# Optimization experiments

Measured on AMD Instinct MI355X. Metric: run time of the kernel, lower is better.

## Reference

```python
import jax, jax.numpy as jnp
import numpy as np

N, E, D, H, L, FF = 50000, 500000, 128, 8, 2, 512
HD = D // H  # head dim = 16


def setup_inputs() -> dict:
    key = jax.random.key(0)
    ks = jax.random.split(key, 16)
    inp = {
        "x": jax.random.normal(ks[0], (N, D), jnp.float32),
        "edge_index": jax.random.randint(ks[1], (2, E), 0, N, jnp.int32),
    }
    def w(k, shape, fan_in):
        return jax.random.normal(k, shape, jnp.float32) / np.float32(np.sqrt(fan_in))
    inp["Wq"] = w(ks[2], (L, D, D), D)
    inp["Wk"] = w(ks[3], (L, D, D), D)
    inp["Wv"] = w(ks[4], (L, D, D), D)
    inp["Wo"] = w(ks[5], (L, D, D), D)
    inp["Wpos"] = w(ks[6], (L, D, D), D)
    inp["Wdeg"] = w(ks[7], (L, 1, D), 1)
    inp["W1"] = w(ks[8], (L, D, FF), D)
    inp["W2"] = w(ks[9], (L, FF, D), FF)
    for name, shape in [("bq", (L, D)), ("bk", (L, D)), ("bv", (L, D)),
                        ("bo", (L, D)), ("bpos", (L, D)), ("bdeg", (L, D)),
                        ("ln1_b", (L, D)), ("ln2_b", (L, D)),
                        ("b1", (L, FF)), ("b2", (L, D))]:
        inp[name] = jnp.zeros(shape, jnp.float32)
    inp["ln1_g"] = jnp.ones((L, D), jnp.float32)
    inp["ln2_g"] = jnp.ones((L, D), jnp.float32)
    return inp


def _layernorm(x, g, b):
    mu = jnp.mean(x, axis=-1, keepdims=True)
    var = jnp.mean(jnp.square(x - mu), axis=-1, keepdims=True)
    return (x - mu) * jax.lax.rsqrt(var + 1e-5) * g + b


def _forward(edge_index, x, Wq, bq, Wk, bk, Wv, bv, Wo, bo, Wpos, bpos,
             Wdeg, bdeg, ln1_g, ln1_b, ln2_g, ln2_b, W1, b1, W2, b2):
    n = x.shape[0]
    loops = jnp.arange(n, dtype=edge_index.dtype)
    src = jnp.concatenate([edge_index[0], loops])  # [E+N]
    dst = jnp.concatenate([edge_index[1], loops])  # [E+N]
    scale = np.float32(np.sqrt(HD))
    for l in range(L):
        # pre-attention LayerNorm
        xn = _layernorm(x, ln1_g[l], ln1_b[l])
        # positional encoding: x + proj(x) + deg_proj(standardized degree)
        deg = jax.ops.segment_sum(jnp.ones_like(src, dtype=x.dtype), src, num_segments=n)
        deg = (deg - deg.mean()) / (jnp.std(deg, ddof=1) + 1e-6)
        pos = xn @ Wpos[l] + bpos[l] + deg[:, None] * Wdeg[l][0] + bdeg[l]
        xp = xn + pos
        # per-node QKV projections (linear => identical to per-edge projection)
        q = (xp @ Wq[l] + bq[l]).reshape(n, H, HD)
        k = (xp @ Wk[l] + bk[l]).reshape(n, H, HD)
        v = (xp @ Wv[l] + bv[l]).reshape(n, H, HD)
        # per-edge attention logits  [E+N, H]
        att = jnp.einsum('ehd,ehd->eh', q[dst], k[src]) / scale
        att = jnp.nan_to_num(jnp.clip(att, -50.0, 50.0), nan=0.0, posinf=50.0, neginf=-50.0)
        # segment softmax over destination nodes (every node has a self loop)
        m = jax.ops.segment_max(att, dst, num_segments=n)        # [N, H]
        ex = jnp.exp(att - m[dst])
        s = jax.ops.segment_sum(ex, dst, num_segments=n)
        alpha = ex / (s[dst] + 1e-16)                             # [E+N, H]
        # weighted aggregation + output projection
        msg = (v[src] * alpha[:, :, None]).reshape(-1, D)         # [E+N, D]
        aggr = jax.ops.segment_sum(msg, dst, num_segments=n)      # [N, D]
        x = x + (aggr @ Wo[l] + bo[l])
        # FFN sublayer
        h = jax.nn.gelu(_layernorm(x, ln2_g[l], ln2_b[l]) @ W1[l] + b1[l], approximate=False)
        x = x + (h @ W2[l] + b2[l])
    return x


def reference(x, edge_index, Wq, bq, Wk, bk, Wv, bv, Wo, bo, Wpos, bpos,
              Wdeg, bdeg, ln1_g, ln1_b, ln2_g, ln2_b, W1, b1, W2, b2):
    return _forward(edge_index, x, Wq, bq, Wk, bk, Wv, bv, Wo, bo, Wpos, bpos,
                    Wdeg, bdeg, ln1_g, ln1_b, ln2_g, ln2_b, W1, b1, W2, b2)
```

## Files before the change

### kernel.cpp

```cpp
#include <hip/hip_runtime.h>
#include <hip/hip_bf16.h>
#include <hip/hip_fp16.h>
#include <math.h>

#define DMODEL 128
#define NHEAD 8
#define HEADD 16
#define NLAYER 2
#define FFDIM 512
#define MPAD 50048
#define QKVW 384
#define CSTRIDE 128
#define LSTR 134

using short8 = __attribute__((ext_vector_type(8))) short;
using half8  = __attribute__((ext_vector_type(8))) _Float16;
using f32x4  = __attribute__((ext_vector_type(4))) float;

static __device__ __forceinline__ unsigned short f2h(float f) {
    __half h = __float2half(f);
    unsigned short u; __builtin_memcpy(&u, &h, 2); return u;
}
static __device__ __forceinline__ float h2f(unsigned short u) {
    __half h; __builtin_memcpy(&h, &u, 2); return __half2float(h);
}
static __device__ __forceinline__ half8 s2h8(short8 s) {
    half8 h; __builtin_memcpy(&h, &s, 16); return h;
}
static __device__ __forceinline__ f32x4 MFMAH(short8 a, short8 b, f32x4 c) {
    return __builtin_amdgcn_mfma_f32_16x16x32_f16(s2h8(a), s2h8(b), c, 0, 0, 0);
}
static __device__ __forceinline__ float gelu_fast(float v) {
    float u = v * (0.7978845608f + 0.0356774081f * v * v);
    float t = 1.0f - 2.0f / (1.0f + __expf(2.0f * u));
    return 0.5f * v * (1.0f + t);
}

__global__ __launch_bounds__(256)
void mega_setup(const int* __restrict__ ei, float* __restrict__ deg,
                int* __restrict__ cnt, int* __restrict__ csr2, int e, int n, int nbT,
                const float* __restrict__ Wq, const float* __restrict__ Wk,
                const float* __restrict__ Wv, const float* __restrict__ Wo,
                const float* __restrict__ Wpos, const float* __restrict__ W1,
                const float* __restrict__ W2,
                unsigned short* __restrict__ wqkvt, unsigned short* __restrict__ wot,
                unsigned short* __restrict__ wpt, unsigned short* __restrict__ w1t,
                unsigned short* __restrict__ w2t, int nbW,
                const float* __restrict__ x_in, const float* __restrict__ g1,
                const float* __restrict__ b1, unsigned short* __restrict__ xnb)
{
    const int bid = blockIdx.x;
    if (bid < nbT) {
        int i = bid * 256 + threadIdx.x;
        if (i < e) {
            int s = ei[i], d = ei[e + i];
            atomicAdd(&deg[s], 1.0f);
            int pos = atomicAdd(&cnt[d], 1);
            if (pos < CSTRIDE) csr2[(size_t)d * CSTRIDE + pos] = s;
        } else if (i < e + n) {
            int d = i - e;
            int pos = atomicAdd(&cnt[d], 1);
            if (pos < CSTRIDE) csr2[(size_t)d * CSTRIDE + pos] = d;
        }
    } else if (bid < nbT + nbW) {
        const int DD = NLAYER * DMODEL * DMODEL;
        const int DF = NLAYER * DMODEL * FFDIM;
        int i = (bid - nbT) * 256 + threadIdx.x;
        if (i < 3 * DD) {
            int w = i / DD, r = i - w * DD;
            const float* src = (w == 0) ? Wq : (w == 1 ? Wk : Wv);
            int l = r >> 14, rr = r & 16383;
            int k = rr >> 7, nn = rr & 127;
            wqkvt[(size_t)l * QKVW * DMODEL + (size_t)(w * 128 + nn) * DMODEL + k] = f2h(src[r]);
        } else if (i < 5 * DD) {
            int w = (i - 3 * DD) / DD, r = (i - 3 * DD) - w * DD;
            const float* src = (w == 0) ? Wo : Wpos;
            unsigned short* dst = (w == 0) ? wot : wpt;
            int l = r >> 14, rr = r & 16383;
            int k = rr >> 7, nn = rr & 127;
            dst[(size_t)l * DMODEL * DMODEL + (size_t)nn * DMODEL + k] = f2h(src[r]);
        } else if (i < 5 * DD + DF) {
            int r = i - 5 * DD;
            int l = r >> 16, rr = r & 65535;
            int k = rr >> 9, nn = rr & 511;
            w1t[(size_t)l * FFDIM * DMODEL + (size_t)nn * DMODEL + k] = f2h(W1[r]);
        } else if (i < 5 * DD + 2 * DF) {
            int r = i - 5 * DD - DF;
            int l = r >> 16, rr = r & 65535;
            int k = rr >> 7, nn = rr & 127;
            w2t[(size_t)l * DMODEL * FFDIM + (size_t)nn * FFDIM + k] = f2h(W2[r]);
        }
    } else {
        int wave = threadIdx.x >> 6;
        int lane = threadIdx.x & 63;
        int row  = (bid - nbT - nbW) * 4 + wave;
        if (row >= n) return;
        float2 xv = *(const float2*)(x_in + (size_t)row * DMODEL + lane * 2);
        float s  = xv.x + xv.y;
        float ss = xv.x * xv.x + xv.y * xv.y;
        #pragma unroll
        for (int d = 1; d < 64; d <<= 1) {
            s  += __shfl_xor(s, d);
            ss += __shfl_xor(ss, d);
        }
        float mu   = s * (1.0f / 128.0f);
        float var  = ss * (1.0f / 128.0f) - mu * mu;
        float rstd = rsqrtf(var + 1e-5f);
        float2 gv = *(const float2*)(g1 + lane * 2);
        float2 bv = *(const float2*)(b1 + lane * 2);
        ushort2 o;
        o.x = f2h((xv.x - mu) * rstd * gv.x + bv.x);
        o.y = f2h((xv.y - mu) * rstd * gv.y + bv.y);
        *(ushort2*)(xnb + (size_t)row * DMODEL + lane * 2) = o;
    }
}

__global__ __launch_bounds__(256)
void deg_var(const float* __restrict__ deg, float* __restrict__ stats, float mean, int n)
{
    float acc = 0.f;
    for (int i = blockIdx.x * blockDim.x + threadIdx.x; i < n; i += gridDim.x * blockDim.x) {
        float d = (deg[i] + 1.0f) - mean;
        acc += d * d;
    }
    #pragma unroll
    for (int d = 1; d < 64; d <<= 1) acc += __shfl_xor(acc, d);
    __shared__ float wsum[4];
    int lane = threadIdx.x & 63, wv = threadIdx.x >> 6;
    if (lane == 0) wsum[wv] = acc;
    __syncthreads();
    if (threadIdx.x == 0) atomicAdd(stats, wsum[0] + wsum[1] + wsum[2] + wsum[3]);
}

static __device__ __forceinline__ void ep_resln(
    f32x4 (&acc)[2][4], float* sm, int row0,
    int wr, int wc, int quad, int l15,
    const float* __restrict__ bias, const float* __restrict__ g,
    const float* __restrict__ bb,
    float* __restrict__ x, unsigned short* __restrict__ lnout, int n)
{
    #pragma unroll
    for (int i = 0; i < 2; ++i) {
        #pragma unroll
        for (int rr = 0; rr < 4; ++rr) {
            int rl = wr * 32 + i * 16 + quad * 4 + rr;
            size_t gr = (size_t)row0 + rl;
            float ps = 0.f, pq = 0.f;
            #pragma unroll
            for (int j = 0; j < 4; ++j) {
                int gc = wc * 64 + j * 16 + l15;
                float xv = (gr < (size_t)n) ? x[gr * DMODEL + gc] : 0.f;
                float v = acc[i][j][rr] + bias[gc] + xv;
                acc[i][j][rr] = v;
                ps += v; pq += v * v;
            }
            ps += __shfl_xor(ps, 1); pq += __shfl_xor(pq, 1);
            ps += __shfl_xor(ps, 2); pq += __shfl_xor(pq, 2);
            ps += __shfl_xor(ps, 4); pq += __shfl_xor(pq, 4);
            ps += __shfl_xor(ps, 8); pq += __shfl_xor(pq, 8);
            if (l15 == 0) { sm[(rl * 2 + wc) * 2 + 0] = ps; sm[(rl * 2 + wc) * 2 + 1] = pq; }
        }
    }
    __syncthreads();
    #pragma unroll
    for (int i = 0; i < 2; ++i) {
        #pragma unroll
        for (int rr = 0; rr < 4; ++rr) {
            int rl = wr * 32 + i * 16 + quad * 4 + rr;
            size_t gr = (size_t)row0 + rl;
            if (gr >= (size_t)n) continue;
            float su = sm[(rl * 2 + 0) * 2 + 0] + sm[(rl * 2 + 1) * 2 + 0];
            float sq = sm[(rl * 2 + 0) * 2 + 1] + sm[(rl * 2 + 1) * 2 + 1];
            float mu   = su * (1.f / 128.f);
            float var  = sq * (1.f / 128.f) - mu * mu;
            float rstd = rsqrtf(var + 1e-5f);
            #pragma unroll
            for (int j = 0; j < 4; ++j) {
                int gc = wc * 64 + j * 16 + l15;
                float v = acc[i][j][rr];
                x[gr * DMODEL + gc] = v;
                lnout[gr * DMODEL + gc] = f2h((v - mu) * rstd * g[gc] + bb[gc]);
            }
        }
    }
}

static __device__ __forceinline__ void ep_resln_lds(
    f32x4 (&acc)[2][4], float* sm, int row0,
    int wr, int wc, int quad, int l15,
    const float* __restrict__ bias, const float* __restrict__ g,
    const float* __restrict__ bb,
    float* __restrict__ x, unsigned short* AsLds, int n)
{
    #pragma unroll
    for (int i = 0; i < 2; ++i) {
        #pragma unroll
        for (int rr = 0; rr < 4; ++rr) {
            int rl = wr * 32 + i * 16 + quad * 4 + rr;
            size_t gr = (size_t)row0 + rl;
            float ps = 0.f, pq = 0.f;
            #pragma unroll
            for (int j = 0; j < 4; ++j) {
                int gc = wc * 64 + j * 16 + l15;
                float xv = (gr < (size_t)n) ? x[gr * DMODEL + gc] : 0.f;
                float v = acc[i][j][rr] + bias[gc] + xv;
                acc[i][j][rr] = v;
                ps += v; pq += v * v;
            }
            ps += __shfl_xor(ps, 1); pq += __shfl_xor(pq, 1);
            ps += __shfl_xor(ps, 2); pq += __shfl_xor(pq, 2);
            ps += __shfl_xor(ps, 4); pq += __shfl_xor(pq, 4);
            ps += __shfl_xor(ps, 8); pq += __shfl_xor(pq, 8);
            if (l15 == 0) { sm[(rl * 2 + wc) * 2 + 0] = ps; sm[(rl * 2 + wc) * 2 + 1] = pq; }
        }
    }
    __syncthreads();
    #pragma unroll
    for (int i = 0; i < 2; ++i) {
        #pragma unroll
        for (int rr = 0; rr < 4; ++rr) {
            int rl = wr * 32 + i * 16 + quad * 4 + rr;
            size_t gr = (size_t)row0 + rl;
            if (gr >= (size_t)n) continue;
            float su = sm[(rl * 2 + 0) * 2 + 0] + sm[(rl * 2 + 1) * 2 + 0];
            float sq = sm[(rl * 2 + 0) * 2 + 1] + sm[(rl * 2 + 1) * 2 + 1];
            float mu   = su * (1.f / 128.f);
            float var  = sq * (1.f / 128.f) - mu * mu;
            float rstd = rsqrtf(var + 1e-5f);
            #pragma unroll
            for (int j = 0; j < 4; ++j) {
                int gc = wc * 64 + j * 16 + l15;
                float v = acc[i][j][rr];
                x[gr * DMODEL + gc] = v;
                AsLds[rl * LSTR + gc] = f2h((v - mu) * rstd * g[gc] + bb[gc]);
            }
        }
    }
}

static __device__ __forceinline__ void panel_load(short8 (&pw)[8],
                                                  const unsigned short* __restrict__ src, int tid)
{
    #pragma unroll
    for (int cc = 0; cc < 8; ++cc) {
        int g = tid + cc * 256; int r = g >> 4, col8 = g & 15;
        pw[cc] = *(const short8*)(src + (size_t)r * DMODEL + col8 * 8);
    }
}
static __device__ __forceinline__ void panel_store(unsigned short* Bs,
                                                   const short8 (&pw)[8], int tid)
{
    #pragma unroll
    for (int cc = 0; cc < 8; ++cc) {
        int g = tid + cc * 256; int r = g >> 4, col8 = g & 15;
        *(short8*)&Bs[r * LSTR + col8 * 8] = pw[cc];
    }
}

__global__ __launch_bounds__(256)
void pos_qkv(const unsigned short* __restrict__ xnb,
             const unsigned short* __restrict__ wpos,
             const unsigned short* __restrict__ wqkv,
             const float* __restrict__ bpos,
             const float* __restrict__ deg, const float* __restrict__ stats, float mean,
             const float* __restrict__ wdeg, const float* __restrict__ bdeg,
             const float* __restrict__ bq, const float* __restrict__ bk,
             const float* __restrict__ bv,
             unsigned short* __restrict__ qkv, int n)
{
    __shared__ __align__(16) unsigned short As[64 * LSTR];
    __shared__ __align__(16) unsigned short Bs[128 * LSTR];

    const int tid = threadIdx.x, wave = tid >> 6, lane = tid & 63;
    const int wr = wave >> 1, wc = wave & 1, quad = lane >> 4, l15 = lane & 15;
    const int row0 = blockIdx.x * 64;

    #pragma unroll
    for (int c = 0; c < 4; ++c) {
        int g = tid + c * 256; int r = g >> 4, col8 = g & 15;
        *(short8*)&As[r * LSTR + col8 * 8] =
            *(const short8*)(xnb + (size_t)(row0 + r) * DMODEL + col8 * 8);
    }
    #pragma unroll
    for (int c = 0; c < 8; ++c) {
        int g = tid + c * 256; int r = g >> 4, col8 = g & 15;
        *(short8*)&Bs[r * LSTR + col8 * 8] =
            *(const short8*)(wpos + (size_t)r * DMODEL + col8 * 8);
    }
    short8 pw[8];
    panel_load(pw, wqkv, tid);
    __syncthreads();

    short8 af[2][4], bfr[4][4];
    #pragma unroll
    for (int i = 0; i < 2; ++i)
        #pragma unroll
        for (int ks = 0; ks < 4; ++ks)
            af[i][ks] = *(const short8*)&As[(wr * 32 + i * 16 + l15) * LSTR + (ks * 4 + quad) * 8];
    #pragma unroll
    for (int j = 0; j < 4; ++j)
        #pragma unroll
        for (int ks = 0; ks < 4; ++ks)
            bfr[j][ks] = *(const short8*)&Bs[(wc * 64 + j * 16 + l15) * LSTR + (ks * 4 + quad) * 8];
    __syncthreads();

    f32x4 acc[2][4] = {};
    #pragma unroll
    for (int ks = 0; ks < 4; ++ks)
        #pragma unroll
        for (int i = 0; i < 2; ++i)
            #pragma unroll
            for (int j = 0; j < 4; ++j)
                acc[i][j] = MFMAH(af[i][ks], bfr[j][ks], acc[i][j]);

    {
        float sdv = sqrtf(stats[0] / (float)(n - 1)) + 1e-6f;
        #pragma unroll
        for (int i = 0; i < 2; ++i) {
            #pragma unroll
            for (int rr = 0; rr < 4; ++rr) {
                int rl = wr * 32 + i * 16 + quad * 4 + rr;
                size_t gr = (size_t)row0 + rl;
                if (gr >= (size_t)n) continue;
                float dg = (deg[gr] + 1.0f - mean) / sdv;
                #pragma unroll
                for (int j = 0; j < 4; ++j) {
                    int gc = wc * 64 + j * 16 + l15;
                    float xn = h2f(As[rl * LSTR + gc]);
                    float val = acc[i][j][rr] + bpos[gc] + dg * wdeg[gc] + bdeg[gc] + xn;
                    As[rl * LSTR + gc] = f2h(val);
                }
            }
        }
    }
    __syncthreads();

    short8 af2[2][4];
    #pragma unroll
    for (int i = 0; i < 2; ++i)
        #pragma unroll
        for (int ks = 0; ks < 4; ++ks)
            af2[i][ks] = *(const short8*)&As[(wr * 32 + i * 16 + l15) * LSTR + (ks * 4 + quad) * 8];
    __syncthreads();

    #pragma unroll
    for (int c = 0; c < 3; ++c) {
        panel_store(Bs, pw, tid);
        if (c < 2) panel_load(pw, wqkv + (size_t)(c + 1) * DMODEL * DMODEL, tid);
        __syncthreads();
        short8 bf2[4][4];
        #pragma unroll
        for (int j = 0; j < 4; ++j)
            #pragma unroll
            for (int ks = 0; ks < 4; ++ks)
                bf2[j][ks] = *(const short8*)&Bs[(wc * 64 + j * 16 + l15) * LSTR + (ks * 4 + quad) * 8];

        f32x4 a2[2][4] = {};
        #pragma unroll
        for (int ks = 0; ks < 4; ++ks)
            #pragma unroll
            for (int i = 0; i < 2; ++i)
                #pragma unroll
                for (int j = 0; j < 4; ++j)
                    a2[i][j] = MFMAH(af2[i][ks], bf2[j][ks], a2[i][j]);

        const float* bp = (c == 0) ? bq : (c == 1 ? bk : bv);
        #pragma unroll
        for (int i = 0; i < 2; ++i) {
            #pragma unroll
            for (int rr = 0; rr < 4; ++rr) {
                size_t gr = (size_t)row0 + wr * 32 + i * 16 + quad * 4 + rr;
                if (gr >= (size_t)n) continue;
                #pragma unroll
                for (int j = 0; j < 4; ++j) {
                    int col = wc * 64 + j * 16 + l15;
                    float val = a2[i][j][rr] + bp[col];
                    int idx = (c == 0) ? col
                            : (128 + ((col >> 1) << 2) + ((c - 1) << 1) + (col & 1));
                    qkv[gr * (size_t)QKVW + idx] = f2h(val);
                }
            }
        }
        if (c < 2) __syncthreads();
    }
}

__global__ __launch_bounds__(256)
void wo_ffn1(const unsigned short* __restrict__ aggr,
             const unsigned short* __restrict__ wo, const float* __restrict__ bo,
             const float* __restrict__ lng, const float* __restrict__ lnb,
             const unsigned short* __restrict__ w1, const float* __restrict__ b1,
             float* __restrict__ x, unsigned short* __restrict__ hb, int n)
{
    __shared__ __align__(16) unsigned short As[64 * LSTR];
    __shared__ __align__(16) unsigned short Bs[128 * LSTR];
    __shared__ float sm[64 * 2 * 2];

    const int tid = threadIdx.x, wave = tid >> 6, lane = tid & 63;
    const int wr = wave >> 1, wc = wave & 1, quad = lane >> 4, l15 = lane & 15;
    const int row0 = blockIdx.x * 64;

    #pragma unroll
    for (int c = 0; c < 4; ++c) {
        int g = tid + c * 256; int r = g >> 4, col8 = g & 15;
        *(short8*)&As[r * LSTR + col8 * 8] =
            *(const short8*)(aggr + (size_t)(row0 + r) * DMODEL + col8 * 8);
    }
    #pragma unroll
    for (int c = 0; c < 8; ++c) {
        int g = tid + c * 256; int r = g >> 4, col8 = g & 15;
        *(short8*)&Bs[r * LSTR + col8 * 8] =
            *(const short8*)(wo + (size_t)r * DMODEL + col8 * 8);
    }
    short8 pw[8];
    panel_load(pw, w1, tid);
    __syncthreads();

    short8 af[2][4], bfr[4][4];
    #pragma unroll
    for (int i = 0; i < 2; ++i)
        #pragma unroll
        for (int ks = 0; ks < 4; ++ks)
            af[i][ks] = *(const short8*)&As[(wr * 32 + i * 16 + l15) * LSTR + (ks * 4 + quad) * 8];
    #pragma unroll
    for (int j = 0; j < 4; ++j)
        #pragma unroll
        for (int ks = 0; ks < 4; ++ks)
            bfr[j][ks] = *(const short8*)&Bs[(wc * 64 + j * 16 + l15) * LSTR + (ks * 4 + quad) * 8];

    f32x4 acc[2][4] = {};
    #pragma unroll
    for (int ks = 0; ks < 4; ++ks)
        #pragma unroll
        for (int i = 0; i < 2; ++i)
            #pragma unroll
            for (int j = 0; j < 4; ++j)
                acc[i][j] = MFMAH(af[i][ks], bfr[j][ks], acc[i][j]);

    ep_resln_lds(acc, sm, row0, wr, wc, quad, l15, bo, lng, lnb, x, As, n);
    __syncthreads();

    short8 af2[2][4];
    #pragma unroll
    for (int i = 0; i < 2; ++i)
        #pragma unroll
        for (int ks = 0; ks < 4; ++ks)
            af2[i][ks] = *(const short8*)&As[(wr * 32 + i * 16 + l15) * LSTR + (ks * 4 + quad) * 8];

    #pragma unroll
    for (int c = 0; c < 4; ++c) {
        panel_store(Bs, pw, tid);
        if (c < 3) panel_load(pw, w1 + (size_t)(c + 1) * 128 * DMODEL, tid);
        __syncthreads();
        short8 bf2[4][4];
        #pragma unroll
        for (int j = 0; j < 4; ++j)
            #pragma unroll
            for (int ks = 0; ks < 4; ++ks)
                bf2[j][ks] = *(const short8*)&Bs[(wc * 64 + j * 16 + l15) * LSTR + (ks * 4 + quad) * 8];

        f32x4 a2[2][4] = {};
        #pragma unroll
        for (int ks = 0; ks < 4; ++ks)
            #pragma unroll
            for (int i = 0; i < 2; ++i)
                #pragma unroll
                for (int j = 0; j < 4; ++j)
                    a2[i][j] = MFMAH(af2[i][ks], bf2[j][ks], a2[i][j]);

        #pragma unroll
        for (int i = 0; i < 2; ++i) {
            #pragma unroll
            for (int rr = 0; rr < 4; ++rr) {
                size_t gr = (size_t)row0 + wr * 32 + i * 16 + quad * 4 + rr;
                if (gr >= (size_t)n) continue;
                #pragma unroll
                for (int j = 0; j < 4; ++j) {
                    int gcol = c * 128 + wc * 64 + j * 16 + l15;
                    float val = gelu_fast(a2[i][j][rr] + b1[gcol]);
                    hb[gr * (size_t)FFDIM + gcol] = f2h(val);
                }
            }
        }
        if (c < 3) __syncthreads();
    }
}

template<int MODE, int KCH>
__global__ __launch_bounds__(256)
void gemm_bres(const unsigned short* __restrict__ A, int strideA,
               const unsigned short* __restrict__ Bt, int strideB,
               const float* __restrict__ bias,
               const float* __restrict__ lng, const float* __restrict__ lnb,
               float* __restrict__ outf, unsigned short* __restrict__ outb,
               int outStride, int n)
{
    __shared__ __align__(16) unsigned short As[64 * LSTR];
    __shared__ __align__(16) unsigned short Bs[128 * LSTR];
    __shared__ float sm[64 * 2 * 2];

    const int tid  = threadIdx.x;
    const int wave = tid >> 6, lane = tid & 63;
    const int wr = wave >> 1, wc = wave & 1;
    const int quad = lane >> 4, l15 = lane & 15;
    const int row0 = blockIdx.x * 64;

    f32x4 acc[2][4] = {};
    short8 pa[4], pb[8];

    #pragma unroll
    for (int c = 0; c < 4; ++c) {
        int g = tid + c * 256;
        int r = g >> 4, col8 = g & 15;
        pa[c] = *(const short8*)(A + (size_t)(row0 + r) * strideA + col8 * 8);
    }
    #pragma unroll
    for (int c = 0; c < 8; ++c) {
        int g = tid + c * 256;
        int r = g >> 4, col8 = g & 15;
        pb[c] = *(const short8*)(Bt + (size_t)r * strideB + col8 * 8);
    }

    for (int ky = 0; ky < KCH; ++ky) {
        #pragma unroll
        for (int c = 0; c < 4; ++c) {
            int g = tid + c * 256;
            int r = g >> 4, col8 = g & 15;
            *(short8*)&As[r * LSTR + col8 * 8] = pa[c];
        }
        #pragma unroll
        for (int c = 0; c < 8; ++c) {
            int g = tid + c * 256;
            int r = g >> 4, col8 = g & 15;
            *(short8*)&Bs[r * LSTR + col8 * 8] = pb[c];
        }
        if (ky + 1 < KCH) {
            const int nkOff = (ky + 1) * 128;
            #pragma unroll
            for (int c = 0; c < 4; ++c) {
                int g = tid + c * 256;
                int r = g >> 4, col8 = g & 15;
                pa[c] = *(const short8*)(A + (size_t)(row0 + r) * strideA + nkOff + col8 * 8);
            }
            #pragma unroll
            for (int c = 0; c < 8; ++c) {
                int g = tid + c * 256;
                int r = g >> 4, col8 = g & 15;
                pb[c] = *(const short8*)(Bt + (size_t)r * strideB + nkOff + col8 * 8);
            }
        }
        __syncthreads();
        short8 af[2][4], bfr[4][4];
        #pragma unroll
        for (int j = 0; j < 4; ++j)
            #pragma unroll
            for (int ks = 0; ks < 4; ++ks)
                bfr[j][ks] = *(const short8*)&Bs[(wc * 64 + j * 16 + l15) * LSTR + (ks * 4 + quad) * 8];
        #pragma unroll
        for (int i = 0; i < 2; ++i)
            #pragma unroll
            for (int ks = 0; ks < 4; ++ks)
                af[i][ks] = *(const short8*)&As[(wr * 32 + i * 16 + l15) * LSTR + (ks * 4 + quad) * 8];
        #pragma unroll
        for (int ks = 0; ks < 4; ++ks)
            #pragma unroll
            for (int i = 0; i < 2; ++i)
                #pragma unroll
                for (int j = 0; j < 4; ++j)
                    acc[i][j] = MFMAH(af[i][ks], bfr[j][ks], acc[i][j]);
        __syncthreads();
    }

    if (MODE == 5) {
        ep_resln(acc, sm, row0, wr, wc, quad, l15, bias, lng, lnb, outf, outb, n);
    } else {
        #pragma unroll
        for (int i = 0; i < 2; ++i) {
            #pragma unroll
            for (int rr = 0; rr < 4; ++rr) {
                size_t gr = (size_t)row0 + wr * 32 + i * 16 + quad * 4 + rr;
                if (gr >= (size_t)n) continue;
                #pragma unroll
                for (int j = 0; j < 4; ++j) {
                    int gc = wc * 64 + j * 16 + l15;
                    float* px = outf + gr * (size_t)outStride + gc;
                    *px = *px + acc[i][j][rr] + bias[gc];
                }
            }
        }
    }
}

__global__ __launch_bounds__(256)
void attn_kernel(const unsigned short* __restrict__ qkv,
                 const int* __restrict__ csr2, const int* __restrict__ cntarr,
                 unsigned short* __restrict__ aggr, int n)
{
    int wave = threadIdx.x >> 6;
    int lane = threadIdx.x & 63;
    int node = blockIdx.x * 4 + wave;
    if (node >= n) return;

    ushort2 qu = *(const ushort2*)(qkv + (size_t)node * QKVW + lane * 2);
    float qx = h2f(qu.x), qy = h2f(qu.y);
    const int* src = csr2 + (size_t)node * CSTRIDE;
    int cnt = cntarr[node];
    if (cnt > CSTRIDE) cnt = CSTRIDE;

    const unsigned short* kvbase = qkv + DMODEL + lane * 4;

    float m = -1e30f, s = 0.f, ax = 0.f, ay = 0.f;
    ushort4 kvA = {0,0,0,0}, kvB = {0,0,0,0};
    int jn0 = 0, jn1 = 0;
    {
        int j0 = src[0];
        kvA = *(const ushort4*)(kvbase + (size_t)j0 * QKVW);
        if (cnt > 1) {
            int j1 = src[1];
            kvB = *(const ushort4*)(kvbase + (size_t)j1 * QKVW);
        }
        if (cnt > 3)      { jn0 = src[2]; jn1 = src[3]; }
        else if (cnt > 2) { jn0 = src[2]; }
    }
    int t = 0;
    for (; t + 1 < cnt; t += 2) {
        ushort4 k0 = kvA, k1 = kvB;
        int rem = cnt - t - 2;
        if (rem >= 2) {
            kvA = *(const ushort4*)(kvbase + (size_t)jn0 * QKVW);
            kvB = *(const ushort4*)(kvbase + (size_t)jn1 * QKVW);
        } else if (rem == 1) {
            kvA = *(const ushort4*)(kvbase + (size_t)jn0 * QKVW);
        }
        if (cnt > t + 5)      { jn0 = src[t + 4]; jn1 = src[t + 5]; }
        else if (cnt > t + 4) { jn0 = src[t + 4]; }
        float p0 = qx * h2f(k0.x) + qy * h2f(k0.y);
        float p1 = qx * h2f(k1.x) + qy * h2f(k1.y);
        p0 += __shfl_xor(p0, 1); p1 += __shfl_xor(p1, 1);
        p0 += __shfl_xor(p0, 2); p1 += __shfl_xor(p1, 2);
        p0 += __shfl_xor(p0, 4); p1 += __shfl_xor(p1, 4);
        p0 *= 0.25f; p1 *= 0.25f;
        p0 = (p0 != p0) ? 0.f : fminf(fmaxf(p0, -50.f), 50.f);
        p1 = (p1 != p1) ? 0.f : fminf(fmaxf(p1, -50.f), 50.f);
        float nm = fmaxf(m, fmaxf(p0, p1));
        float sc = __expf(m - nm);
        float e0 = __expf(p0 - nm), e1 = __expf(p1 - nm);
        s  = s  * sc + e0 + e1;
        ax = ax * sc + e0 * h2f(k0.z) + e1 * h2f(k1.z);
        ay = ay * sc + e0 * h2f(k0.w) + e1 * h2f(k1.w);
        m = nm;
    }
    if (t < cnt) {
        float p0 = qx * h2f(kvA.x) + qy * h2f(kvA.y);
        p0 += __shfl_xor(p0, 1); p0 += __shfl_xor(p0, 2); p0 += __shfl_xor(p0, 4);
        p0 *= 0.25f;
        p0 = (p0 != p0) ? 0.f : fminf(fmaxf(p0, -50.f), 50.f);
        float nm = fmaxf(m, p0);
        float sc = __expf(m - nm), e0 = __expf(p0 - nm);
        s = s * sc + e0;
        ax = ax * sc + e0 * h2f(kvA.z);
        ay = ay * sc + e0 * h2f(kvA.w);
        m = nm;
    }
    float r = 1.0f / (s + 1e-16f);
    ushort2 o;
    o.x = f2h(ax * r);
    o.y = f2h(ay * r);
    *(ushort2*)(aggr + (size_t)node * DMODEL + lane * 2) = o;
}

extern "C" void kernel_launch(void* const* d_in, const int* in_sizes, int n_in,
                              void* d_out, int out_size, void* d_ws, size_t ws_size,
                              hipStream_t stream)
{
    const float* x_in  = (const float*)d_in[0];
    const int*   ei    = (const int*)d_in[1];
    const float* Wq    = (const float*)d_in[2];
    const float* Wk    = (const float*)d_in[3];
    const float* Wv    = (const float*)d_in[4];
    const float* Wo    = (const float*)d_in[5];
    const float* Wpos  = (const float*)d_in[6];
    const float* Wdeg  = (const float*)d_in[7];
    const float* W1    = (const float*)d_in[8];
    const float* W2    = (const float*)d_in[9];
    const float* bq    = (const float*)d_in[10];
    const float* bk    = (const float*)d_in[11];
    const float* bv    = (const float*)d_in[12];
    const float* bo    = (const float*)d_in[13];
    const float* bpos  = (const float*)d_in[14];
    const float* bdeg  = (const float*)d_in[15];
    const float* ln1_b = (const float*)d_in[16];
    const float* ln2_b = (const float*)d_in[17];
    const float* b1    = (const float*)d_in[18];
    const float* b2    = (const float*)d_in[19];
    const float* ln1_g = (const float*)d_in[20];
    const float* ln2_g = (const float*)d_in[21];

    const int n   = in_sizes[0] / DMODEL;
    const int e   = in_sizes[1] / 2;
    const int tot = e + n;

    float* x = (float*)d_out;

    char* p = (char*)d_ws;
    auto alloc = [&](size_t bytes) -> void* {
        void* r = (void*)p;
        p += (bytes + 255) & ~(size_t)255;
        return r;
    };
    float* deg     = (float*)alloc((size_t)n * 4);
    float* stats   = (float*)alloc(256);
    int*   cnt     = (int*)alloc((size_t)n * 4);
    int*   csr2    = (int*)alloc((size_t)MPAD * CSTRIDE * 4);
    unsigned short* xnb  = (unsigned short*)alloc((size_t)MPAD * DMODEL * 2);
    unsigned short* aggr = (unsigned short*)alloc((size_t)MPAD * DMODEL * 2);
    unsigned short* qkv  = (unsigned short*)alloc((size_t)MPAD * QKVW * 2);
    unsigned short* hb   = (unsigned short*)alloc((size_t)MPAD * FFDIM * 2);
    unsigned short* wqkvt = (unsigned short*)alloc((size_t)NLAYER * QKVW * DMODEL * 2);
    unsigned short* wot  = (unsigned short*)alloc((size_t)NLAYER * DMODEL * DMODEL * 2);
    unsigned short* wpt  = (unsigned short*)alloc((size_t)NLAYER * DMODEL * DMODEL * 2);
    unsigned short* w1t  = (unsigned short*)alloc((size_t)NLAYER * DMODEL * FFDIM * 2);
    unsigned short* w2t  = (unsigned short*)alloc((size_t)NLAYER * FFDIM * DMODEL * 2);

    const int nbT = (tot + 255) / 256;
    const int nbW = (5 * NLAYER * DMODEL * DMODEL + 2 * NLAYER * DMODEL * FFDIM + 255) / 256;
    const int lnB = (n + 3) / 4;

    hipMemcpyAsync(x, x_in, (size_t)n * DMODEL * 4, hipMemcpyDeviceToDevice, stream);
    hipMemsetAsync(deg, 0, (size_t)((char*)(cnt + n) - (char*)deg), stream);

    mega_setup<<<nbT + nbW + lnB, 256, 0, stream>>>(
        ei, deg, cnt, csr2, e, n, nbT,
        Wq, Wk, Wv, Wo, Wpos, W1, W2,
        wqkvt, wot, wpt, w1t, w2t, nbW,
        x_in, ln1_g, ln1_b, xnb);

    const float mean = (float)((double)tot / (double)n);
    deg_var<<<196, 256, 0, stream>>>(deg, stats, mean, n);

    const int nTiles = MPAD / 64;
    const int ln_grid = (n + 3) / 4;

    for (int l = 0; l < NLAYER; ++l) {
        const size_t DD = (size_t)DMODEL * DMODEL;
        const float* wdeg = Wdeg + (size_t)l * DMODEL;
        const unsigned short* wqkv = wqkvt + (size_t)l * QKVW * DMODEL;
        const unsigned short* wo   = wot + l * DD;
        const unsigned short* wpos = wpt + l * DD;
        const unsigned short* w1   = w1t + (size_t)l * DMODEL * FFDIM;
        const unsigned short* w2   = w2t + (size_t)l * FFDIM * DMODEL;

        pos_qkv<<<nTiles, 256, 0, stream>>>(
            xnb, wpos, wqkv,
            bpos + l * DMODEL, deg, stats, mean, wdeg, bdeg + l * DMODEL,
            bq + l * DMODEL, bk + l * DMODEL, bv + l * DMODEL,
            qkv, n);
        attn_kernel<<<ln_grid, 256, 0, stream>>>(qkv, csr2, cnt, aggr, n);
        wo_ffn1<<<nTiles, 256, 0, stream>>>(
            aggr, wo, bo + l * DMODEL,
            ln2_g + l * DMODEL, ln2_b + l * DMODEL,
            w1, b1 + l * FFDIM,
            x, hb, n);
        if (l + 1 < NLAYER) {
            gemm_bres<5, 4><<<dim3(nTiles, 1), 256, 0, stream>>>(
                hb, FFDIM, w2, FFDIM,
                b2 + l * DMODEL,
                ln1_g + (l + 1) * DMODEL, ln1_b + (l + 1) * DMODEL,
                x, xnb, DMODEL, n);
        } else {
            gemm_bres<1, 4><<<dim3(nTiles, 1), 256, 0, stream>>>(
                hb, FFDIM, w2, FFDIM,
                b2 + l * DMODEL,
                nullptr, nullptr,
                x, nullptr, DMODEL, n);
        }
    }
}
```

Before: 550.6 us.

## Drop initial x copy and remove register prefetch of weight panels

```diff
diff --git a/kernel.cpp b/kernel.cpp
--- a/kernel.cpp
+++ b/kernel.cpp
@@ -137,7 +137,8 @@
     int wr, int wc, int quad, int l15,
     const float* __restrict__ bias, const float* __restrict__ g,
     const float* __restrict__ bb,
-    float* __restrict__ x, unsigned short* __restrict__ lnout, int n)
+    const float* __restrict__ xin, float* __restrict__ x,
+    unsigned short* __restrict__ lnout, int n)
 {
     #pragma unroll
     for (int i = 0; i < 2; ++i) {
@@ -149,7 +150,7 @@
             #pragma unroll
             for (int j = 0; j < 4; ++j) {
                 int gc = wc * 64 + j * 16 + l15;
-                float xv = (gr < (size_t)n) ? x[gr * DMODEL + gc] : 0.f;
+                float xv = (gr < (size_t)n) ? xin[gr * DMODEL + gc] : 0.f;
                 float v = acc[i][j][rr] + bias[gc] + xv;
                 acc[i][j][rr] = v;
                 ps += v; pq += v * v;
@@ -190,7 +191,8 @@
     int wr, int wc, int quad, int l15,
     const float* __restrict__ bias, const float* __restrict__ g,
     const float* __restrict__ bb,
-    float* __restrict__ x, unsigned short* AsLds, int n)
+    const float* __restrict__ xin, float* __restrict__ x,
+    unsigned short* AsLds, int n)
 {
     #pragma unroll
     for (int i = 0; i < 2; ++i) {
@@ -202,7 +204,7 @@
             #pragma unroll
             for (int j = 0; j < 4; ++j) {
                 int gc = wc * 64 + j * 16 + l15;
-                float xv = (gr < (size_t)n) ? x[gr * DMODEL + gc] : 0.f;
+                float xv = (gr < (size_t)n) ? xin[gr * DMODEL + gc] : 0.f;
                 float v = acc[i][j][rr] + bias[gc] + xv;
                 acc[i][j][rr] = v;
                 ps += v; pq += v * v;
@@ -235,25 +237,6 @@
                 AsLds[rl * LSTR + gc] = f2h((v - mu) * rstd * g[gc] + bb[gc]);
             }
         }
-    }
-}
-
-static __device__ __forceinline__ void panel_load(short8 (&pw)[8],
-                                                  const unsigned short* __restrict__ src, int tid)
-{
-    #pragma unroll
-    for (int cc = 0; cc < 8; ++cc) {
-        int g = tid + cc * 256; int r = g >> 4, col8 = g & 15;
-        pw[cc] = *(const short8*)(src + (size_t)r * DMODEL + col8 * 8);
-    }
-}
-static __device__ __forceinline__ void panel_store(unsigned short* Bs,
-                                                   const short8 (&pw)[8], int tid)
-{
-    #pragma unroll
-    for (int cc = 0; cc < 8; ++cc) {
-        int g = tid + cc * 256; int r = g >> 4, col8 = g & 15;
-        *(short8*)&Bs[r * LSTR + col8 * 8] = pw[cc];
     }
 }
 
@@ -287,8 +270,6 @@
         *(short8*)&Bs[r * LSTR + col8 * 8] =
             *(const short8*)(wpos + (size_t)r * DMODEL + col8 * 8);
     }
-    short8 pw[8];
-    panel_load(pw, wqkv, tid);
     __syncthreads();
 
     short8 af[2][4], bfr[4][4];
@@ -345,8 +326,12 @@
 
     #pragma unroll
     for (int c = 0; c < 3; ++c) {
-        panel_store(Bs, pw, tid);
-        if (c < 2) panel_load(pw, wqkv + (size_t)(c + 1) * DMODEL * DMODEL, tid);
+        #pragma unroll
+        for (int cc = 0; cc < 8; ++cc) {
+            int g = tid + cc * 256; int r = g >> 4, col8 = g & 15;
+            *(short8*)&Bs[r * LSTR + col8 * 8] =
+                *(const short8*)(wqkv + (size_t)(c * 128 + r) * DMODEL + col8 * 8);
+        }
         __syncthreads();
         short8 bf2[4][4];
         #pragma unroll
@@ -390,7 +375,8 @@
              const unsigned short* __restrict__ wo, const float* __restrict__ bo,
              const float* __restrict__ lng, const float* __restrict__ lnb,
              const unsigned short* __restrict__ w1, const float* __restrict__ b1,
-             float* __restrict__ x, unsigned short* __restrict__ hb, int n)
+             const float* __restrict__ xres, float* __restrict__ x,
+             unsigned short* __restrict__ hb, int n)
 {
     __shared__ __align__(16) unsigned short As[64 * LSTR];
     __shared__ __align__(16) unsigned short Bs[128 * LSTR];
@@ -412,8 +398,6 @@
         *(short8*)&Bs[r * LSTR + col8 * 8] =
             *(const short8*)(wo + (size_t)r * DMODEL + col8 * 8);
     }
-    short8 pw[8];
-    panel_load(pw, w1, tid);
     __syncthreads();
 
     short8 af[2][4], bfr[4][4];
@@ -437,7 +421,7 @@
             for (int j = 0; j < 4; ++j)
                 acc[i][j] = MFMAH(af[i][ks], bfr[j][ks], acc[i][j]);
 
-    ep_resln_lds(acc, sm, row0, wr, wc, quad, l15, bo, lng, lnb, x, As, n);
+    ep_resln_lds(acc, sm, row0, wr, wc, quad, l15, bo, lng, lnb, xres, x, As, n);
     __syncthreads();
 
     short8 af2[2][4];
@@ -449,8 +433,12 @@
 
     #pragma unroll
     for (int c = 0; c < 4; ++c) {
-        panel_store(Bs, pw, tid);
-        if (c < 3) panel_load(pw, w1 + (size_t)(c + 1) * 128 * DMODEL, tid);
+        #pragma unroll
+        for (int cc = 0; cc < 8; ++cc) {
+            int g = tid + cc * 256; int r = g >> 4, col8 = g & 15;
+            *(short8*)&Bs[r * LSTR + col8 * 8] =
+                *(const short8*)(w1 + (size_t)(c * 128 + r) * DMODEL + col8 * 8);
+        }
         __syncthreads();
         short8 bf2[4][4];
         #pragma unroll
@@ -506,7 +494,7 @@
     const int row0 = blockIdx.x * 64;
 
     f32x4 acc[2][4] = {};
-    short8 pa[4], pb[8];
+    short8 pa[4];
 
     #pragma unroll
     for (int c = 0; c < 4; ++c) {
@@ -514,26 +502,22 @@
         int r = g >> 4, col8 = g & 15;
         pa[c] = *(const short8*)(A + (size_t)(row0 + r) * strideA + col8 * 8);
     }
-    #pragma unroll
-    for (int c = 0; c < 8; ++c) {
-        int g = tid + c * 256;
-        int r = g >> 4, col8 = g & 15;
-        pb[c] = *(const short8*)(Bt + (size_t)r * strideB + col8 * 8);
-    }
 
     for (int ky = 0; ky < KCH; ++ky) {
+        const int kOff = ky * 128;
+        #pragma unroll
+        for (int c = 0; c < 8; ++c) {
+            int g = tid + c * 256;
+            int r = g >> 4, col8 = g & 15;
+            *(short8*)&Bs[r * LSTR + col8 * 8] =
+                *(const short8*)(Bt + (size_t)r * strideB + kOff + col8 * 8);
+        }
         #pragma unroll
         for (int c = 0; c < 4; ++c) {
             int g = tid + c * 256;
             int r = g >> 4, col8 = g & 15;
             *(short8*)&As[r * LSTR + col8 * 8] = pa[c];
         }
-        #pragma unroll
-        for (int c = 0; c < 8; ++c) {
-            int g = tid + c * 256;
-            int r = g >> 4, col8 = g & 15;
-            *(short8*)&Bs[r * LSTR + col8 * 8] = pb[c];
-        }
         if (ky + 1 < KCH) {
             const int nkOff = (ky + 1) * 128;
             #pragma unroll
@@ -541,12 +525,6 @@
                 int g = tid + c * 256;
                 int r = g >> 4, col8 = g & 15;
                 pa[c] = *(const short8*)(A + (size_t)(row0 + r) * strideA + nkOff + col8 * 8);
-            }
-            #pragma unroll
-            for (int c = 0; c < 8; ++c) {
-                int g = tid + c * 256;
-                int r = g >> 4, col8 = g & 15;
-                pb[c] = *(const short8*)(Bt + (size_t)r * strideB + nkOff + col8 * 8);
             }
         }
         __syncthreads();
@@ -572,7 +550,7 @@
     }
 
     if (MODE == 5) {
-        ep_resln(acc, sm, row0, wr, wc, quad, l15, bias, lng, lnb, outf, outb, n);
+        ep_resln(acc, sm, row0, wr, wc, quad, l15, bias, lng, lnb, outf, outf, outb, n);
     } else {
         #pragma unroll
         for (int i = 0; i < 2; ++i) {
@@ -726,7 +704,6 @@
     const int nbW = (5 * NLAYER * DMODEL * DMODEL + 2 * NLAYER * DMODEL * FFDIM + 255) / 256;
     const int lnB = (n + 3) / 4;
 
-    hipMemcpyAsync(x, x_in, (size_t)n * DMODEL * 4, hipMemcpyDeviceToDevice, stream);
     hipMemsetAsync(deg, 0, (size_t)((char*)(cnt + n) - (char*)deg), stream);
 
     mega_setup<<<nbT + nbW + lnB, 256, 0, stream>>>(
@@ -760,7 +737,7 @@
             aggr, wo, bo + l * DMODEL,
             ln2_g + l * DMODEL, ln2_b + l * DMODEL,
             w1, b1 + l * FFDIM,
-            x, hb, n);
+            (l == 0) ? x_in : x, x, hb, n);
         if (l + 1 < NLAYER) {
             gemm_bres<5, 4><<<dim3(nTiles, 1), 256, 0, stream>>>(
                 hb, FFDIM, w2, FFDIM,
```

New measurement: 506.4 us. -8.0%, faster.
